# Kernel tuning notes

Measured on AMD Instinct MI355X. Metric: run time of the kernel, lower is better.

Reference implementation:

```python
import jax, jax.numpy as jnp
import numpy as np

N, C, G, H = 64, 23, 20000, 64  # batch, NB_CHROM, NB_GENES, HIDDEN


def setup_inputs() -> dict:
    key = jax.random.key(0)
    k1, k2, k3 = jax.random.split(key, 3)
    x = jax.random.normal(k1, (N, G, H), dtype=jnp.float32)
    # each gene belongs to exactly one chromosome -> one-hot composition matrix (C, G)
    assign = jax.random.randint(k2, (G,), 0, C)
    chrom_mat = jax.nn.one_hot(assign, C, dtype=jnp.float32).T  # (C, G)
    attention = jax.random.normal(k3, (C, H), dtype=jnp.float32)
    return {"x": x, "chrom_mat": chrom_mat, "attention": attention}


def reference(x, chrom_mat, attention):
    # Original: h = einsum('ij,njk->nijk', mask, x); att = einsum('ij,kijm->kim', A, h.transpose(2,3))
    # Algebraically identical fused form: att[n,i,g] = mask[i,g] * <A[i,:], x[n,g,:]>
    att = jnp.einsum('ih,ngh->nig', attention, x) * chrom_mat[None]  # (N, C, G)
    mask = (att != 0).astype(att.dtype)  # mask = att.bool().byte()
    att = jnp.exp(jax.nn.leaky_relu(att, negative_slope=0.2)) * mask
    att = att / jnp.maximum(att.sum(axis=2, keepdims=True), jnp.float32(1e-10))
    return jnp.einsum('nig,ngh->nih', att, x)  # bmm(att, x) -> (N, C, H)
```

## Files before the change

kernel.cpp:

```cpp
#include <hip/hip_runtime.h>
#include <hip/hip_bf16.h>

#define N_ 64
#define C_ 23
#define G_ 20000
#define H_ 64
#define S_ 4

__global__ void assign_kernel(const float* __restrict__ chrom,
                              int* __restrict__ assign,
                              int* __restrict__ counts) {
    int g = blockIdx.x * blockDim.x + threadIdx.x;
    if (g >= G_) return;
    int c_found = 0;
    for (int c = 0; c < C_; ++c) {
        if (chrom[c * G_ + g] != 0.f) c_found = c;
    }
    assign[g] = c_found;
    atomicAdd(&counts[c_found], 1);
}

__global__ void scan_kernel(const int* __restrict__ counts,
                            int* __restrict__ offsets,
                            int* __restrict__ cursors) {
    if (threadIdx.x == 0 && blockIdx.x == 0) {
        int run = 0;
        for (int c = 0; c < C_; ++c) {
            offsets[c] = run;
            cursors[c] = run;
            run += counts[c];
        }
        offsets[C_] = run;
    }
}

__global__ void scatter_kernel(const int* __restrict__ assign,
                               int* __restrict__ cursors,
                               int* __restrict__ sorted_g) {
    int g = blockIdx.x * blockDim.x + threadIdx.x;
    if (g >= G_) return;
    int c = assign[g];
    int pos = atomicAdd(&cursors[c], 1);
    sorted_g[pos] = g;
}

__global__ __launch_bounds__(256) void main_pass(
    const float* __restrict__ x,
    const float* __restrict__ attn,
    const int* __restrict__ offsets,
    const int* __restrict__ sorted_g,
    float* __restrict__ acc,
    float* __restrict__ denom)
{
    int b = blockIdx.x;
    int s = b % S_; b /= S_;
    int c = b % C_; b /= C_;
    int n = b;

    int beg = offsets[c];
    int end = offsets[c + 1];
    int cnt = end - beg;
    int L   = (cnt + S_ - 1) / S_;
    int lo  = beg + s * L;
    int hi  = min(beg + (s + 1) * L, end);

    int tid = threadIdx.x;
    int sub = tid & 15;
    int grp = tid >> 4;

    const float4 a4 = ((const float4*)(attn + c * H_))[sub];

    float4 accv = make_float4(0.f, 0.f, 0.f, 0.f);
    float dsum = 0.f;

    for (int p = lo + grp; p < hi; p += 16) {
        int g = sorted_g[p];
        const float4 x4 = ((const float4*)(x + ((size_t)n * G_ + g) * H_))[sub];
        float part = a4.x * x4.x + a4.y * x4.y + a4.z * x4.z + a4.w * x4.w;
        part += __shfl_xor(part, 1);
        part += __shfl_xor(part, 2);
        part += __shfl_xor(part, 4);
        part += __shfl_xor(part, 8);
        float w;
        if (part == 0.f) {
            w = 0.f;
        } else {
            float lr = (part >= 0.f) ? part : 0.2f * part;
            w = __expf(lr);
        }
        accv.x += w * x4.x;
        accv.y += w * x4.y;
        accv.z += w * x4.z;
        accv.w += w * x4.w;
        dsum += w;
    }

    #pragma unroll
    for (int m = 16; m <= 32; m <<= 1) {
        accv.x += __shfl_xor(accv.x, m);
        accv.y += __shfl_xor(accv.y, m);
        accv.z += __shfl_xor(accv.z, m);
        accv.w += __shfl_xor(accv.w, m);
        dsum   += __shfl_xor(dsum, m);
    }

    int lane = tid & 63;
    float* accp = acc + ((size_t)n * C_ + c) * H_;
    if (lane < 16) {
        atomicAdd(accp + sub * 4 + 0, accv.x);
        atomicAdd(accp + sub * 4 + 1, accv.y);
        atomicAdd(accp + sub * 4 + 2, accv.z);
        atomicAdd(accp + sub * 4 + 3, accv.w);
        if (sub == 0) atomicAdd(denom + n * C_ + c, dsum);
    }
}

__global__ void finalize_kernel(const float* __restrict__ acc,
                                const float* __restrict__ denom,
                                float* __restrict__ out) {
    int i = blockIdx.x * blockDim.x + threadIdx.x;
    if (i >= N_ * C_ * H_) return;
    int nc = i >> 6;
    float d = fmaxf(denom[nc], 1e-10f);
    out[i] = acc[i] / d;
}

extern "C" void kernel_launch(void* const* d_in, const int* in_sizes, int n_in,
                              void* d_out, int out_size, void* d_ws, size_t ws_size,
                              hipStream_t stream) {
    const float* x     = (const float*)d_in[0];
    const float* chrom = (const float*)d_in[1];
    const float* attn  = (const float*)d_in[2];
    float* out = (float*)d_out;

    float* acc    = (float*)d_ws;
    float* denom  = acc + (size_t)N_ * C_ * H_;
    int*   counts  = (int*)(denom + (size_t)N_ * C_);
    int*   cursors = counts + C_;
    int*   offsets = cursors + C_;
    int*   assign  = offsets + (C_ + 1);
    int*   sorted  = assign + G_;

    size_t zero_bytes = ((size_t)N_ * C_ * H_ + (size_t)N_ * C_ + 2 * C_) * sizeof(float);
    hipMemsetAsync(d_ws, 0, zero_bytes, stream);

    int gb = (G_ + 255) / 256;
    assign_kernel<<<gb, 256, 0, stream>>>(chrom, assign, counts);
    scan_kernel<<<1, 64, 0, stream>>>(counts, offsets, cursors);
    scatter_kernel<<<gb, 256, 0, stream>>>(assign, cursors, sorted);

    int main_blocks = N_ * C_ * S_;
    main_pass<<<main_blocks, 256, 0, stream>>>(x, attn, offsets, sorted, acc, denom);

    int fin_blocks = (N_ * C_ * H_ + 255) / 256;
    finalize_kernel<<<fin_blocks, 256, 0, stream>>>(acc, denom, out);
}
```

Baseline: 535.7 us.

## Stream genes contiguously and accumulate per-chromosome sums in shared memory

```diff
diff --git a/kernel.cpp b/kernel.cpp
--- a/kernel.cpp
+++ b/kernel.cpp
@@ -5,113 +5,79 @@
 #define C_ 23
 #define G_ 20000
 #define H_ 64
-#define S_ 4
+#define SLICES 32
+#define GPB ((G_ + SLICES - 1) / SLICES)
 
 __global__ void assign_kernel(const float* __restrict__ chrom,
-                              int* __restrict__ assign,
-                              int* __restrict__ counts) {
+                              int* __restrict__ assign) {
     int g = blockIdx.x * blockDim.x + threadIdx.x;
     if (g >= G_) return;
     int c_found = 0;
+    #pragma unroll
     for (int c = 0; c < C_; ++c) {
         if (chrom[c * G_ + g] != 0.f) c_found = c;
     }
     assign[g] = c_found;
-    atomicAdd(&counts[c_found], 1);
 }
 
-__global__ void scan_kernel(const int* __restrict__ counts,
-                            int* __restrict__ offsets,
-                            int* __restrict__ cursors) {
-    if (threadIdx.x == 0 && blockIdx.x == 0) {
-        int run = 0;
-        for (int c = 0; c < C_; ++c) {
-            offsets[c] = run;
-            cursors[c] = run;
-            run += counts[c];
-        }
-        offsets[C_] = run;
-    }
-}
-
-__global__ void scatter_kernel(const int* __restrict__ assign,
-                               int* __restrict__ cursors,
-                               int* __restrict__ sorted_g) {
-    int g = blockIdx.x * blockDim.x + threadIdx.x;
-    if (g >= G_) return;
-    int c = assign[g];
-    int pos = atomicAdd(&cursors[c], 1);
-    sorted_g[pos] = g;
-}
-
-__global__ __launch_bounds__(256) void main_pass(
+__global__ __launch_bounds__(256) void main_stream(
     const float* __restrict__ x,
     const float* __restrict__ attn,
-    const int* __restrict__ offsets,
-    const int* __restrict__ sorted_g,
+    const int* __restrict__ assign,
     float* __restrict__ acc,
     float* __restrict__ denom)
 {
-    int b = blockIdx.x;
-    int s = b % S_; b /= S_;
-    int c = b % C_; b /= C_;
-    int n = b;
+    __shared__ float attn_s[C_ * H_];
+    __shared__ float acc_s[C_ * H_];
+    __shared__ float den_s[C_];
 
-    int beg = offsets[c];
-    int end = offsets[c + 1];
-    int cnt = end - beg;
-    int L   = (cnt + S_ - 1) / S_;
-    int lo  = beg + s * L;
-    int hi  = min(beg + (s + 1) * L, end);
+    int n = blockIdx.x / SLICES;
+    int s = blockIdx.x % SLICES;
+    int lo = s * GPB;
+    int hi = min(lo + GPB, G_);
 
     int tid = threadIdx.x;
+    for (int i = tid; i < C_ * H_; i += 256) {
+        attn_s[i] = attn[i];
+        acc_s[i]  = 0.f;
+    }
+    if (tid < C_) den_s[tid] = 0.f;
+    __syncthreads();
+
     int sub = tid & 15;
     int grp = tid >> 4;
 
-    const float4 a4 = ((const float4*)(attn + c * H_))[sub];
-
-    float4 accv = make_float4(0.f, 0.f, 0.f, 0.f);
-    float dsum = 0.f;
-
-    for (int p = lo + grp; p < hi; p += 16) {
-        int g = sorted_g[p];
+    for (int g = lo + grp; g < hi; g += 16) {
+        int c = assign[g];
         const float4 x4 = ((const float4*)(x + ((size_t)n * G_ + g) * H_))[sub];
+        const float4 a4 = ((const float4*)(attn_s + c * H_))[sub];
         float part = a4.x * x4.x + a4.y * x4.y + a4.z * x4.z + a4.w * x4.w;
         part += __shfl_xor(part, 1);
         part += __shfl_xor(part, 2);
         part += __shfl_xor(part, 4);
         part += __shfl_xor(part, 8);
-        float w;
-        if (part == 0.f) {
-            w = 0.f;
-        } else {
+        float w = 0.f;
+        if (part != 0.f) {
             float lr = (part >= 0.f) ? part : 0.2f * part;
             w = __expf(lr);
         }
-        accv.x += w * x4.x;
-        accv.y += w * x4.y;
-        accv.z += w * x4.z;
-        accv.w += w * x4.w;
-        dsum += w;
+        float* ap = acc_s + c * H_ + sub * 4;
+        unsafeAtomicAdd(ap + 0, w * x4.x);
+        unsafeAtomicAdd(ap + 1, w * x4.y);
+        unsafeAtomicAdd(ap + 2, w * x4.z);
+        unsafeAtomicAdd(ap + 3, w * x4.w);
+        if (sub == 0) unsafeAtomicAdd(&den_s[c], w);
     }
+    __syncthreads();
 
-    #pragma unroll
-    for (int m = 16; m <= 32; m <<= 1) {
-        accv.x += __shfl_xor(accv.x, m);
-        accv.y += __shfl_xor(accv.y, m);
-        accv.z += __shfl_xor(accv.z, m);
-        accv.w += __shfl_xor(accv.w, m);
-        dsum   += __shfl_xor(dsum, m);
+    float* accg = acc + (size_t)n * C_ * H_;
+    for (int i = tid; i < C_ * H_; i += 256) {
+        float v = acc_s[i];
+        if (v != 0.f) unsafeAtomicAdd(accg + i, v);
     }
-
-    int lane = tid & 63;
-    float* accp = acc + ((size_t)n * C_ + c) * H_;
-    if (lane < 16) {
-        atomicAdd(accp + sub * 4 + 0, accv.x);
-        atomicAdd(accp + sub * 4 + 1, accv.y);
-        atomicAdd(accp + sub * 4 + 2, accv.z);
-        atomicAdd(accp + sub * 4 + 3, accv.w);
-        if (sub == 0) atomicAdd(denom + n * C_ + c, dsum);
+    if (tid < C_) {
+        float v = den_s[tid];
+        if (v != 0.f) unsafeAtomicAdd(denom + n * C_ + tid, v);
     }
 }
 
@@ -135,23 +101,14 @@
 
     float* acc    = (float*)d_ws;
     float* denom  = acc + (size_t)N_ * C_ * H_;
-    int*   counts  = (int*)(denom + (size_t)N_ * C_);
-    int*   cursors = counts + C_;
-    int*   offsets = cursors + C_;
-    int*   assign  = offsets + (C_ + 1);
-    int*   sorted  = assign + G_;
+    int*   assign = (int*)(denom + (size_t)N_ * C_);
 
-    size_t zero_bytes = ((size_t)N_ * C_ * H_ + (size_t)N_ * C_ + 2 * C_) * sizeof(float);
+    size_t zero_bytes = ((size_t)N_ * C_ * H_ + (size_t)N_ * C_) * sizeof(float);
     hipMemsetAsync(d_ws, 0, zero_bytes, stream);
 
-    int gb = (G_ + 255) / 256;
-    assign_kernel<<<gb, 256, 0, stream>>>(chrom, assign, counts);
-    scan_kernel<<<1, 64, 0, stream>>>(counts, offsets, cursors);
-    scatter_kernel<<<gb, 256, 0, stream>>>(assign, cursors, sorted);
+    assign_kernel<<<(G_ + 255) / 256, 256, 0, stream>>>(chrom, assign);
 
-    int main_blocks = N_ * C_ * S_;
-    main_pass<<<main_blocks, 256, 0, stream>>>(x, attn, offsets, sorted, acc, denom);
+    main_stream<<<N_ * SLICES, 256, 0, stream>>>(x, attn, assign, acc, denom);
 
-    int fin_blocks = (N_ * C_ * H_ + 255) / 256;
-    finalize_kernel<<<fin_blocks, 256, 0, stream>>>(acc, denom, out);
+    finalize_kernel<<<(N_ * C_ * H_ + 255) / 256, 256, 0, stream>>>(acc, denom, out);
 }
```

Result: slower. 755.5 us (+41.0%).
